# Kernel tuning notes

Measured on AMD Instinct MI355X. Metric: run time of the kernel, lower is better.

The kernel has to match this reference:

```python
import jax, jax.numpy as jnp
import numpy as np

B, S, H, P, D = 4, 2048, 2048, 4096, 1024
I = min(1024, P)  # intermediate_dim


def setup_inputs() -> dict:
    key = jax.random.key(0)
    ks = jax.random.split(key, 8)
    sc = lambda n: 1.0 / np.sqrt(n)
    return {
        "x": jax.random.normal(ks[0], (B, S, H), jnp.float32),
        "tensor_pool": jax.random.normal(ks[1], (P, D), jnp.float32),
        "top_k": 2,
        "w1": jax.random.normal(ks[2], (H, I), jnp.float32) * sc(H),
        "b1": jnp.zeros((I,), jnp.float32),
        "w2": jax.random.normal(ks[3], (I, P), jnp.float32) * sc(I),
        "b2": jnp.zeros((P,), jnp.float32),
        "temperature": jnp.float32(0.5),
        "wp": jax.random.normal(ks[4], (H, D), jnp.float32) * sc(H),
        "bp": jnp.zeros((D,), jnp.float32),
        "gamma": jnp.ones((D,), jnp.float32),
        "beta": jnp.zeros((D,), jnp.float32),
        "wm": jax.random.normal(ks[5], (2 * D, D), jnp.float32) * sc(2 * D),
        "bm": jnp.zeros((D,), jnp.float32),
    }


def _layer_norm(h, gamma, beta, eps=1e-5):
    mu = jnp.mean(h, axis=-1, keepdims=True)
    var = jnp.mean(jnp.square(h - mu), axis=-1, keepdims=True)
    return (h - mu) * jax.lax.rsqrt(var + eps) * gamma + beta


def reference(x, tensor_pool, top_k, w1, b1, w2, b2, temperature, wp, bp, gamma, beta, wm, bm):
    pool_size = tensor_pool.shape[0]
    # router MLP
    inter = jax.nn.relu(jnp.einsum('bsh,hi->bsi', x, w1) + b1)
    logits = jnp.einsum('bsi,ip->bsp', inter, w2) + b2
    temp = jnp.clip(temperature, 0.1, 5.0)
    scaled_logits = jnp.clip(logits / temp, -10.0, 10.0)
    # top-k select + softmax over selected
    topk_logits, topk_idx = jax.lax.top_k(scaled_logits, top_k)  # [B,S,K]
    topk_w = jax.nn.softmax(topk_logits, axis=-1)
    # gather pool entries and combine
    experts_out = tensor_pool[topk_idx]                     # [B,S,K,D]
    weighted_map = jnp.einsum('bsk,bskd->bsd', topk_w, experts_out)
    projected_x = _layer_norm(jnp.einsum('bsh,hd->bsd', x, wp) + bp, gamma, beta)
    combined = jnp.concatenate([projected_x, weighted_map], axis=-1)  # [B,S,2D]
    transformation = jnp.einsum('bse,ed->bsd', combined, wm) + bm
    # usage stats via scatter-add
    usage = jnp.zeros((pool_size,), x.dtype).at[topk_idx.reshape(-1)].add(topk_w.reshape(-1))
    usage_fraction = usage / (usage.sum() + 1e-8)
    uniform = 1.0 / pool_size
    scale = min(1.0, x.size / (pool_size * top_k))
    diversity_loss = jnp.mean(jnp.square(usage_fraction - uniform)) * scale * 0.01
    return transformation, diversity_loss
```

## Files before the change

kernel.cpp:

```cpp
#include <hip/hip_runtime.h>
#include <hip/hip_bf16.h>
#include <float.h>
#include <limits.h>

#define NTOK 8192
#define H_   2048
#define P_   4096
#define D_   1024
#define I_   1024

#define MAXC  16
#define DELTA 0.09375f
#define TAU   4.0e-4f
#define FLAGCAP 512

typedef unsigned short ushort_t;
typedef __attribute__((ext_vector_type(8))) short short8;
typedef __attribute__((ext_vector_type(4))) float floatx4;

static __device__ inline ushort_t f2bf(float f) {
    __hip_bfloat16 h = __float2bfloat16(f);
    return *reinterpret_cast<ushort_t*>(&h);
}
static __device__ inline short f2bfs(float f) {
    __hip_bfloat16 h = __float2bfloat16(f);
    return *reinterpret_cast<short*>(&h);
}
static __device__ inline float bf2f(ushort_t s) { return __uint_as_float((unsigned)s << 16); }

static __device__ inline void ins2(float& v0, int& i0, float& v1, int& i1, float v, int i) {
    if (v > v0 || (v == v0 && i < i0)) { v1 = v0; i1 = i0; v0 = v; i0 = i; }
    else if (v > v1 || (v == v1 && i < i1)) { v1 = v; i1 = i; }
}

static __device__ __forceinline__ void gload16(const void* g, void* l) {
    __builtin_amdgcn_global_load_lds(
        (const __attribute__((address_space(1))) unsigned int*)g,
        (__attribute__((address_space(3))) unsigned int*)l,
        16, 0, 0);
}

__global__ __launch_bounds__(256) void prep_weights(
    const float* __restrict__ w2, float* __restrict__ w2tf, ushort_t* __restrict__ w2t,
    const float* __restrict__ wp, ushort_t* __restrict__ wpt,
    const float* __restrict__ wm, ushort_t* __restrict__ wmt,
    const float* __restrict__ w1, ushort_t* __restrict__ w1tHi, ushort_t* __restrict__ w1tLo)
{
    __shared__ float tile[32][33];
    const int tid = threadIdx.x;
    const int tx = tid & 31, ty = tid >> 5;
    int b = blockIdx.x;
    const float* in; int R, Cc, seg, bx, by;
    if (b < 4096)      { seg = 0; in = w2; R = I_; Cc = P_; bx = b & 127; by = b >> 7; }
    else if (b < 6144) { seg = 1; b -= 4096; in = wp; R = H_; Cc = D_; bx = b & 31; by = b >> 5; }
    else if (b < 8192) { seg = 2; b -= 6144; in = wm; R = H_; Cc = D_; bx = b & 31; by = b >> 5; }
    else               { seg = 3; b -= 8192; in = w1; R = H_; Cc = I_; bx = b & 31; by = b >> 5; }
    const int c0 = bx * 32, r0 = by * 32;
#pragma unroll
    for (int j = 0; j < 4; j++)
        tile[ty + j * 8][tx] = in[(size_t)(r0 + ty + j * 8) * Cc + c0 + tx];
    __syncthreads();
#pragma unroll
    for (int j = 0; j < 4; j++) {
        float v = tile[tx][ty + j * 8];
        const size_t o = (size_t)(c0 + ty + j * 8) * R + r0 + tx;
        if (seg == 0)      { w2t[o] = f2bf(v); w2tf[o] = v; }
        else if (seg == 1) { wpt[o] = f2bf(v); }
        else if (seg == 2) { wmt[o] = f2bf(v); }
        else { ushort_t h = f2bf(v); w1tHi[o] = h; w1tLo[o] = f2bf(v - bf2f(h)); }
    }
}

static __device__ __forceinline__ void stage_slot(
    const ushort_t* __restrict__ base, int ld, int r0, int kt, int p,
    ushort_t* __restrict__ lds)
{
    const int row = p >> 2;
    const int chunk = (p ^ (p >> 2)) & 3;
    gload16(base + (size_t)(r0 + row) * ld + kt * 32 + chunk * 8, lds + p * 8);
}

template<int EPI>
__global__ __launch_bounds__(512, 2) void gemm_pipe(
    const ushort_t* __restrict__ A, int lda,
    const ushort_t* __restrict__ Bt, int ldb,
    const float* __restrict__ bias,
    float* __restrict__ Cf, ushort_t* __restrict__ Cb, int ldc, int K)
{
    __shared__ ushort_t sA[3][256 * 32];
    __shared__ ushort_t sB[3][128 * 32];

    const int tid  = threadIdx.x;
    const int wave = tid >> 6, lane = tid & 63;
    const int lr = lane & 15, lq = lane >> 4;
    const int wrow = wave >> 1, wcol = wave & 1;

    const int nwg = gridDim.x * gridDim.y;
    int bid = blockIdx.y * gridDim.x + blockIdx.x;
    bid = (bid & 7) * (nwg >> 3) + (bid >> 3);
    const int bx = bid % gridDim.x, by = bid / gridDim.x;
    const int m0 = by * 256, n0 = bx * 128;
    const int NT = K >> 5;

    floatx4 acc[4][4] = {};

    stage_slot(A,  lda, m0, 0, tid,       &sA[0][0]);
    stage_slot(A,  lda, m0, 0, tid + 512, &sA[0][0]);
    stage_slot(Bt, ldb, n0, 0, tid,       &sB[0][0]);
    stage_slot(A,  lda, m0, 1, tid,       &sA[1][0]);
    stage_slot(A,  lda, m0, 1, tid + 512, &sA[1][0]);
    stage_slot(Bt, ldb, n0, 1, tid,       &sB[1][0]);

    for (int kt = 0; kt < NT; kt++) {
        const int cb = kt % 3;
        const int sbuf = (kt + 2) % 3;
        const bool st = (kt + 2) < NT;
        const ushort_t* __restrict__ sAc = &sA[cb][0];
        const ushort_t* __restrict__ sBc = &sB[cb][0];
        short8 bF[4];

#pragma unroll
        for (int p = 0; p < 2; p++) {
            if (p == 0) {
                if (kt + 1 < NT) asm volatile("s_waitcnt vmcnt(3)" ::: "memory");
                else             asm volatile("s_waitcnt vmcnt(0)" ::: "memory");
            }
            __builtin_amdgcn_s_barrier();
            short8 aF[2];
#pragma unroll
            for (int t = 0; t < 2; t++) {
                const int row = wrow * 64 + (2 * p + t) * 16 + lr;
                const int ph = row * 4 + (lq ^ (row & 3));
                aF[t] = *(const short8*)&sAc[ph * 8];
            }
            if (p == 0) {
#pragma unroll
                for (int f = 0; f < 4; f++) {
                    const int row = wcol * 64 + f * 16 + lr;
                    const int ph = row * 4 + (lq ^ (row & 3));
                    bF[f] = *(const short8*)&sBc[ph * 8];
                }
            }
            if (st) {
                if (p == 0) {
                    stage_slot(A,  lda, m0, kt + 2, tid, &sA[sbuf][0]);
                    stage_slot(Bt, ldb, n0, kt + 2, tid, &sB[sbuf][0]);
                } else {
                    stage_slot(A,  lda, m0, kt + 2, tid + 512, &sA[sbuf][0]);
                }
            }
            __builtin_amdgcn_s_setprio(1);
#pragma unroll
            for (int t = 0; t < 2; t++)
#pragma unroll
                for (int j = 0; j < 4; j++)
                    acc[2 * p + t][j] = __builtin_amdgcn_mfma_f32_16x16x32_bf16(
                        aF[t], bF[j], acc[2 * p + t][j], 0, 0, 0);
            __builtin_amdgcn_s_setprio(0);
        }
    }

#pragma unroll
    for (int j = 0; j < 4; j++) {
        const int col = n0 + wcol * 64 + j * 16 + lr;
        const float bv = bias[col];
#pragma unroll
        for (int i = 0; i < 4; i++) {
            const int rowb = m0 + wrow * 64 + i * 16 + lq * 4;
#pragma unroll
            for (int r = 0; r < 4; r++) {
                float v = acc[i][j][r] + bv;
                if (EPI == 1) Cb[(size_t)(rowb + r) * ldc + col] = f2bf(v);
                else          Cf[(size_t)(rowb + r) * ldc + col] = v;
            }
        }
    }
}

template<int ASRC, int EPI>
__global__ __launch_bounds__(256) void gemm_lds(
    const void* __restrict__ Av, int lda,
    const ushort_t* __restrict__ Bt, int ldb,
    const float* __restrict__ bias,
    float* __restrict__ Cf, ushort_t* __restrict__ Cb, int ldc, int K)
{
    __shared__ ushort_t sA[128 * 32];
    __shared__ ushort_t sB[128 * 32];

    const int tid  = threadIdx.x;
    const int wave = tid >> 6, lane = tid & 63;
    const int lr = lane & 15, lq = lane >> 4;

    const int nwg = gridDim.x * gridDim.y;
    int bid = blockIdx.y * gridDim.x + blockIdx.x;
    bid = (bid & 7) * (nwg >> 3) + (bid >> 3);
    const int bx = bid % gridDim.x, by = bid / gridDim.x;
    const int m0 = by * 128, n0 = bx * 128;
    const int m0w = m0 + (wave >> 1) * 64, n0w = n0 + (wave & 1) * 64;

    const int n1 = tid, n2 = tid + 256;

    floatx4 acc[4][4] = {};

    for (int k0 = 0; k0 < K; k0 += 32) {
        __syncthreads();
        gload16(Bt + (size_t)(n0 + (n1 >> 2)) * ldb + k0 + (n1 & 3) * 8, &sB[n1 * 8]);
        gload16(Bt + (size_t)(n0 + (n2 >> 2)) * ldb + k0 + (n2 & 3) * 8, &sB[n2 * 8]);
        if (ASRC == 1) {
            const ushort_t* Ab = (const ushort_t*)Av;
            gload16(Ab + (size_t)(m0 + (n1 >> 2)) * lda + k0 + (n1 & 3) * 8, &sA[n1 * 8]);
            gload16(Ab + (size_t)(m0 + (n2 >> 2)) * lda + k0 + (n2 & 3) * 8, &sA[n2 * 8]);
        } else {
#pragma unroll
            for (int ss = 0; ss < 2; ss++) {
                const int s = tid + ss * 256;
                const float* ap = (const float*)Av + (size_t)(m0 + (s >> 2)) * lda + k0 + (s & 3) * 8;
                float4 v0 = *(const float4*)ap;
                float4 v1 = *(const float4*)(ap + 4);
                short8 h;
                h[0] = f2bfs(v0.x); h[1] = f2bfs(v0.y); h[2] = f2bfs(v0.z); h[3] = f2bfs(v0.w);
                h[4] = f2bfs(v1.x); h[5] = f2bfs(v1.y); h[6] = f2bfs(v1.z); h[7] = f2bfs(v1.w);
                *(short8*)&sA[s * 8] = h;
            }
        }
        __syncthreads();

        short8 aF[4], bF[4];
#pragma unroll
        for (int f = 0; f < 4; f++) {
            const int ra = ((wave >> 1) * 64 + f * 16 + lr) * 32 + lq * 8;
            aF[f] = *(const short8*)&sA[ra];
            const int rb = ((wave & 1) * 64 + f * 16 + lr) * 32 + lq * 8;
            bF[f] = *(const short8*)&sB[rb];
        }
#pragma unroll
        for (int i = 0; i < 4; i++)
#pragma unroll
            for (int j = 0; j < 4; j++)
                acc[i][j] = __builtin_amdgcn_mfma_f32_16x16x32_bf16(aF[i], bF[j], acc[i][j], 0, 0, 0);
    }

#pragma unroll
    for (int j = 0; j < 4; j++) {
        const int col = n0w + j * 16 + lr;
        const float bv = bias[col];
#pragma unroll
        for (int i = 0; i < 4; i++) {
            const int rowb = m0w + i * 16 + lq * 4;
#pragma unroll
            for (int r = 0; r < 4; r++) {
                float v = acc[i][j][r] + bv;
                if (EPI == 1) Cb[(size_t)(rowb + r) * ldc + col] = f2bf(v);
                else          Cf[(size_t)(rowb + r) * ldc + col] = v;
            }
        }
    }
}

__global__ __launch_bounds__(256) void gemm_lds_split(
    const float* __restrict__ A, int lda,
    const ushort_t* __restrict__ BtH, const ushort_t* __restrict__ BtL, int ldb,
    const float* __restrict__ bias,
    float* __restrict__ Cf, ushort_t* __restrict__ Cb, int ldc, int K)
{
    __shared__ ushort_t sAh[128 * 32];
    __shared__ ushort_t sAl[128 * 32];
    __shared__ ushort_t sBh[128 * 32];
    __shared__ ushort_t sBl[128 * 32];

    const int tid  = threadIdx.x;
    const int wave = tid >> 6, lane = tid & 63;
    const int lr = lane & 15, lq = lane >> 4;

    const int nwg = gridDim.x * gridDim.y;
    int bid = blockIdx.y * gridDim.x + blockIdx.x;
    bid = (bid & 7) * (nwg >> 3) + (bid >> 3);
    const int bx = bid % gridDim.x, by = bid / gridDim.x;
    const int m0 = by * 128, n0 = bx * 128;
    const int m0w = m0 + (wave >> 1) * 64, n0w = n0 + (wave & 1) * 64;

    const int n1 = tid, n2 = tid + 256;

    floatx4 acc[4][4] = {};

    for (int k0 = 0; k0 < K; k0 += 32) {
        __syncthreads();
        gload16(BtH + (size_t)(n0 + (n1 >> 2)) * ldb + k0 + (n1 & 3) * 8, &sBh[n1 * 8]);
        gload16(BtH + (size_t)(n0 + (n2 >> 2)) * ldb + k0 + (n2 & 3) * 8, &sBh[n2 * 8]);
        gload16(BtL + (size_t)(n0 + (n1 >> 2)) * ldb + k0 + (n1 & 3) * 8, &sBl[n1 * 8]);
        gload16(BtL + (size_t)(n0 + (n2 >> 2)) * ldb + k0 + (n2 & 3) * 8, &sBl[n2 * 8]);
#pragma unroll
        for (int ss = 0; ss < 2; ss++) {
            const int s = tid + ss * 256;
            const float* ap = A + (size_t)(m0 + (s >> 2)) * lda + k0 + (s & 3) * 8;
            float4 v0 = *(const float4*)ap;
            float4 v1 = *(const float4*)(ap + 4);
            float fb[8] = {v0.x, v0.y, v0.z, v0.w, v1.x, v1.y, v1.z, v1.w};
            short8 h, l;
#pragma unroll
            for (int e = 0; e < 8; e++) {
                short hh = f2bfs(fb[e]);
                h[e] = hh; l[e] = f2bfs(fb[e] - bf2f((ushort_t)hh));
            }
            *(short8*)&sAh[s * 8] = h;
            *(short8*)&sAl[s * 8] = l;
        }
        __syncthreads();

        short8 aH[4], aL[4], bH[4], bL[4];
#pragma unroll
        for (int f = 0; f < 4; f++) {
            const int ra = ((wave >> 1) * 64 + f * 16 + lr) * 32 + lq * 8;
            aH[f] = *(const short8*)&sAh[ra];
            aL[f] = *(const short8*)&sAl[ra];
            const int rb = ((wave & 1) * 64 + f * 16 + lr) * 32 + lq * 8;
            bH[f] = *(const short8*)&sBh[rb];
            bL[f] = *(const short8*)&sBl[rb];
        }
#pragma unroll
        for (int i = 0; i < 4; i++)
#pragma unroll
            for (int j = 0; j < 4; j++) {
                acc[i][j] = __builtin_amdgcn_mfma_f32_16x16x32_bf16(aH[i], bH[j], acc[i][j], 0, 0, 0);
                acc[i][j] = __builtin_amdgcn_mfma_f32_16x16x32_bf16(aH[i], bL[j], acc[i][j], 0, 0, 0);
                acc[i][j] = __builtin_amdgcn_mfma_f32_16x16x32_bf16(aL[i], bH[j], acc[i][j], 0, 0, 0);
            }
    }

#pragma unroll
    for (int j = 0; j < 4; j++) {
        const int col = n0w + j * 16 + lr;
        const float bv = bias[col];
#pragma unroll
        for (int i = 0; i < 4; i++) {
            const int rowb = m0w + i * 16 + lq * 4;
#pragma unroll
            for (int r = 0; r < 4; r++) {
                float v = fmaxf(acc[i][j][r] + bv, 0.f);
                Cf[(size_t)(rowb + r) * ldc + col] = v;
                Cb[(size_t)(rowb + r) * ldc + col] = f2bf(v);
            }
        }
    }
}

__global__ __launch_bounds__(256) void cand_scan(
    const ushort_t* __restrict__ logitsb,
    int* __restrict__ cidx, int* __restrict__ ccnt)
{
    __shared__ float sv0[4], sv1[4];
    __shared__ int   scnt;
    const int tok = blockIdx.x;
    const int tid = threadIdx.x;
    const ushort_t* row = logitsb + (size_t)tok * P_;

    float my[16];
    {
        const uint4* rp = (const uint4*)(row + tid * 16);
        uint4 u0 = rp[0], u1 = rp[1];
        unsigned w[8] = {u0.x, u0.y, u0.z, u0.w, u1.x, u1.y, u1.z, u1.w};
#pragma unroll
        for (int j = 0; j < 8; j++) {
            my[2 * j]     = __uint_as_float(w[j] << 16);
            my[2 * j + 1] = __uint_as_float(w[j] & 0xFFFF0000u);
        }
    }
    float v0 = -FLT_MAX, v1 = -FLT_MAX;
#pragma unroll
    for (int j = 0; j < 16; j++) {
        float v = my[j];
        if (v > v0) { v1 = v0; v0 = v; } else if (v > v1) v1 = v;
    }
#pragma unroll
    for (int off = 1; off < 64; off <<= 1) {
        float u0 = __shfl_xor(v0, off), u1 = __shfl_xor(v1, off);
        float n0 = fmaxf(v0, u0);
        float n1 = fmaxf(fminf(v0, u0), fmaxf(v1, u1));
        v0 = n0; v1 = n1;
    }
    const int wv = tid >> 6;
    if ((tid & 63) == 0) { sv0[wv] = v0; sv1[wv] = v1; }
    if (tid == 0) scnt = 0;
    __syncthreads();
    float g0 = -FLT_MAX, g1 = -FLT_MAX;
#pragma unroll
    for (int w = 0; w < 4; w++) {
        float u0 = sv0[w], u1 = sv1[w];
        float n0 = fmaxf(g0, u0);
        float n1 = fmaxf(fminf(g0, u0), fmaxf(g1, u1));
        g0 = n0; g1 = n1;
    }
    const float thresh = g1 - DELTA;
#pragma unroll
    for (int j = 0; j < 16; j++) {
        if (my[j] >= thresh) {
            int pos = atomicAdd(&scnt, 1);
            if (pos < MAXC) cidx[tok * MAXC + pos] = tid * 16 + j;
        }
    }
    __syncthreads();
    if (tid == 0) ccnt[tok] = min(scnt, MAXC);
}

__global__ __launch_bounds__(256) void recheck(
    const float* __restrict__ interf, const float* __restrict__ w2tf,
    const float* __restrict__ b2, const int* __restrict__ cidx,
    const int* __restrict__ ccnt, const float* __restrict__ temp_p,
    int2* __restrict__ tki, float2* __restrict__ tkw,
    int* __restrict__ flagcnt, int* __restrict__ flaglist)
{
    __shared__ double ex[MAXC];
    __shared__ int    sidx[MAXC];
    const int tok  = blockIdx.x;
    const int tid  = threadIdx.x;
    const int wave = tid >> 6, lane = tid & 63;
    int cnt = min(max(ccnt[tok], 0), MAXC);

    const float* ir = interf + (size_t)tok * I_;
    for (int c = wave; c < cnt; c += 4) {
        int p = min(max(cidx[tok * MAXC + c], 0), P_ - 1);
        const float* wr = w2tf + (size_t)p * I_;
        double s = 0.0;
        for (int k = lane; k < I_; k += 64)
            s += (double)ir[k] * (double)wr[k];
#pragma unroll
        for (int off = 32; off; off >>= 1) s += __shfl_down(s, off);
        if (lane == 0) { ex[c] = s + (double)b2[p]; sidx[c] = p; }
    }
    __syncthreads();
    if (tid == 0) {
        float v0 = -FLT_MAX, v1 = -FLT_MAX; int i0 = INT_MAX, i1 = INT_MAX;
        for (int c = 0; c < cnt; c++) ins2(v0, i0, v1, i1, (float)ex[c], sidx[c]);
        if (i0 == INT_MAX) { i0 = 0; v0 = 0.f; }
        if (i1 == INT_MAX) { i1 = i0; v1 = v0; }
        if (cnt >= 3) {
            float v2 = -FLT_MAX;
            for (int c = 0; c < cnt; c++) {
                if (sidx[c] == i0 || sidx[c] == i1) continue;
                float v = (float)ex[c];
                if (v > v2) v2 = v;
            }
            if (v1 - v2 < TAU) {
                int pos = atomicAdd(flagcnt, 1);
                if (pos < FLAGCAP) flaglist[pos] = tok;
            }
        }
        float tc = fminf(fmaxf(temp_p[0], 0.1f), 5.0f);
        float s0 = fminf(fmaxf(v0 / tc, -10.f), 10.f);
        float s1 = fminf(fmaxf(v1 / tc, -10.f), 10.f);
        float m  = fmaxf(s0, s1);
        float e0 = expf(s0 - m), e1 = expf(s1 - m);
        float inv = 1.0f / (e0 + e1);
        tki[tok] = make_int2(i0, i1);
        tkw[tok] = make_float2(e0 * inv, e1 * inv);
    }
}

__global__ __launch_bounds__(256) void fallback_gemv(
    const float* __restrict__ x, const float* __restrict__ w1,
    const int* __restrict__ flagcnt, const int* __restrict__ flaglist,
    double* __restrict__ part)
{
    __shared__ float sx[128];
    const int tid = threadIdx.x;
    const int nf = min(flagcnt[0], FLAGCAP);
    const int nitems = nf * 16;

    for (int idx = blockIdx.x; idx < nitems; idx += gridDim.x) {
        const int fi = idx >> 4, slice = idx & 15;
        const int tok = flaglist[fi];
        const int h0 = slice * 128;
        __syncthreads();
        if (tid < 128) sx[tid] = x[(size_t)tok * H_ + h0 + tid];
        __syncthreads();

        const int col = tid * 4;
        double a0 = 0.0, a1 = 0.0, a2 = 0.0, a3 = 0.0;
        for (int h = 0; h < 128; h += 8) {
            float4 wv[8];
#pragma unroll
            for (int u = 0; u < 8; u++)
                wv[u] = *(const float4*)(w1 + (size_t)(h0 + h + u) * I_ + col);
#pragma unroll
            for (int u = 0; u < 8; u++) {
                const double xv = (double)sx[h + u];
                a0 += xv * (double)wv[u].x;
                a1 += xv * (double)wv[u].y;
                a2 += xv * (double)wv[u].z;
                a3 += xv * (double)wv[u].w;
            }
        }
        double* pp = part + ((size_t)fi * 16 + slice) * I_ + col;
        pp[0] = a0; pp[1] = a1; pp[2] = a2; pp[3] = a3;
    }
}

__global__ __launch_bounds__(256) void fallback_reduce(
    const double* __restrict__ part, const float* __restrict__ b1,
    const float* __restrict__ w2tf, const float* __restrict__ b2,
    const int* __restrict__ cidx, const int* __restrict__ ccnt,
    const int* __restrict__ flagcnt, const int* __restrict__ flaglist,
    const float* __restrict__ temp_p,
    int2* __restrict__ tki, float2* __restrict__ tkw)
{
    __shared__ double sInter[I_];
    __shared__ double ex[MAXC];
    __shared__ int    sidx[MAXC];
    const int tid  = threadIdx.x;
    const int wave = tid >> 6, lane = tid & 63;
    const int nf = min(flagcnt[0], FLAGCAP);

    for (int fi = blockIdx.x; fi < nf; fi += gridDim.x) {
        const int tok = flaglist[fi];
        __syncthreads();
#pragma unroll
        for (int q = 0; q < 4; q++) {
            const int i = q * 256 + tid;
            double v = (double)b1[i];
            const double* pp = part + (size_t)fi * 16 * I_ + i;
#pragma unroll
            for (int s = 0; s < 16; s++) v += pp[(size_t)s * I_];
            sInter[i] = v > 0.0 ? v : 0.0;
        }
        __syncthreads();

        const int cnt = min(max(ccnt[tok], 0), MAXC);
        for (int c = wave; c < cnt; c += 4) {
            int p = min(max(cidx[tok * MAXC + c], 0), P_ - 1);
            const float* wr = w2tf + (size_t)p * I_;
            double s = 0.0;
            for (int k = lane; k < I_; k += 64)
                s += sInter[k] * (double)wr[k];
#pragma unroll
            for (int off = 32; off; off >>= 1) s += __shfl_down(s, off);
            if (lane == 0) { ex[c] = s + (double)b2[p]; sidx[c] = p; }
        }
        __syncthreads();
        if (tid == 0) {
            float v0 = -FLT_MAX, v1 = -FLT_MAX; int i0 = INT_MAX, i1 = INT_MAX;
            for (int c = 0; c < cnt; c++) ins2(v0, i0, v1, i1, (float)ex[c], sidx[c]);
            if (i0 == INT_MAX) { i0 = 0; v0 = 0.f; }
            if (i1 == INT_MAX) { i1 = i0; v1 = v0; }
            float tc = fminf(fmaxf(temp_p[0], 0.1f), 5.0f);
            float s0 = fminf(fmaxf(v0 / tc, -10.f), 10.f);
            float s1 = fminf(fmaxf(v1 / tc, -10.f), 10.f);
            float m  = fmaxf(s0, s1);
            float e0 = expf(s0 - m), e1 = expf(s1 - m);
            float inv = 1.0f / (e0 + e1);
            tki[tok] = make_int2(i0, i1);
            tkw[tok] = make_float2(e0 * inv, e1 * inv);
        }
    }
}

static __device__ inline float blockReduceSum256(float v, float* red) {
#pragma unroll
    for (int off = 32; off; off >>= 1) v += __shfl_down(v, off);
    const int wv = threadIdx.x >> 6;
    if ((threadIdx.x & 63) == 0) red[wv] = v;
    __syncthreads();
    float tot = red[0] + red[1] + red[2] + red[3];
    __syncthreads();
    return tot;
}

__global__ __launch_bounds__(256) void build_combined(
    const float* __restrict__ proj, ushort_t* __restrict__ comb,
    const float* __restrict__ pool,
    const float* __restrict__ gamma, const float* __restrict__ beta,
    const int2* __restrict__ tki, const float2* __restrict__ tkw,
    float* __restrict__ usage)
{
    __shared__ float red[4];
    const int tok = blockIdx.x;
    const int tid = threadIdx.x;
    const int c = tid * 4;

    float4 v = *(const float4*)&proj[(size_t)tok * D_ + c];
    float s = v.x + v.y + v.z + v.w;
    float tot = blockReduceSum256(s, red);
    float mu = tot * (1.0f / D_);
    float d0 = v.x - mu, d1 = v.y - mu, d2 = v.z - mu, d3 = v.w - mu;
    float sq = d0 * d0 + d1 * d1 + d2 * d2 + d3 * d3;
    float var = blockReduceSum256(sq, red) * (1.0f / D_);
    float rs = 1.0f / sqrtf(var + 1e-5f);

    float4 g  = *(const float4*)&gamma[c];
    float4 be = *(const float4*)&beta[c];
    ushort4 o;
    o.x = f2bf(d0 * rs * g.x + be.x);
    o.y = f2bf(d1 * rs * g.y + be.y);
    o.z = f2bf(d2 * rs * g.z + be.z);
    o.w = f2bf(d3 * rs * g.w + be.w);
    *(ushort4*)&comb[(size_t)tok * (2 * D_) + c] = o;

    int2   ii = tki[tok];
    int ia = min(max(ii.x, 0), P_ - 1);
    int ib = min(max(ii.y, 0), P_ - 1);
    float2 ww = tkw[tok];
    float4 p0 = *(const float4*)&pool[(size_t)ia * D_ + c];
    float4 p1 = *(const float4*)&pool[(size_t)ib * D_ + c];
    ushort4 wm;
    wm.x = f2bf(ww.x * p0.x + ww.y * p1.x);
    wm.y = f2bf(ww.x * p0.y + ww.y * p1.y);
    wm.z = f2bf(ww.x * p0.z + ww.y * p1.z);
    wm.w = f2bf(ww.x * p0.w + ww.y * p1.w);
    *(ushort4*)&comb[(size_t)tok * (2 * D_) + D_ + c] = wm;

    if (tid == 0) {
        atomicAdd(&usage[ia], ww.x);
        atomicAdd(&usage[ib], ww.y);
    }
}

__global__ __launch_bounds__(256) void diversity_kernel(
    const float* __restrict__ usage, float* __restrict__ out)
{
    __shared__ float red[4];
    const int tid = threadIdx.x;
    float s = 0.f;
    for (int j = tid; j < P_; j += 256) s += usage[j];
    float tot = blockReduceSum256(s, red) + 1e-8f;
    float q = 0.f;
    const float uni = 1.0f / P_;
    for (int j = tid; j < P_; j += 256) {
        float f = usage[j] / tot - uni;
        q += f * f;
    }
    float ssq = blockReduceSum256(q, red);
    if (tid == 0) out[(size_t)NTOK * D_] = ssq * (1.0f / P_) * 0.01f;
}

extern "C" void kernel_launch(void* const* d_in, const int* in_sizes, int n_in,
                              void* d_out, int out_size, void* d_ws, size_t ws_size,
                              hipStream_t stream) {
    const float* x     = (const float*)d_in[0];
    const float* pool  = (const float*)d_in[1];
    const float* w1    = (const float*)d_in[3];
    const float* b1    = (const float*)d_in[4];
    const float* w2    = (const float*)d_in[5];
    const float* b2    = (const float*)d_in[6];
    const float* temp  = (const float*)d_in[7];
    const float* wp    = (const float*)d_in[8];
    const float* bp    = (const float*)d_in[9];
    const float* gamma = (const float*)d_in[10];
    const float* beta  = (const float*)d_in[11];
    const float* wm    = (const float*)d_in[12];
    const float* bm    = (const float*)d_in[13];
    float* out = (float*)d_out;

    float* ws = (float*)d_ws;
    const size_t MF = (size_t)1024 * 1024;
    float*    interf  = ws;
    ushort_t* interb  = (ushort_t*)(ws + 8 * MF);
    ushort_t* logitsb = (ushort_t*)(ws + 12 * MF);
    double*   part    = (double*)(ws + 12 * MF);
    float*    projb   = ws + 12 * MF;
    ushort_t* comb    = (ushort_t*)(ws + 20 * MF);
    float*    w2tf    = ws + 28 * MF;
    ushort_t* w2t     = (ushort_t*)(ws + 32 * MF);
    ushort_t* wpt     = (ushort_t*)(ws + 34 * MF);
    ushort_t* wmt     = (ushort_t*)(ws + 35 * MF);
    ushort_t* w1tHi   = (ushort_t*)(ws + 36 * MF);
    ushort_t* w1tLo   = (ushort_t*)(ws + 37 * MF);
    int*      cidx    = (int*)(ws + 38 * MF);
    int*      ccnt    = cidx + NTOK * MAXC;
    int2*     tki     = (int2*)(ccnt + NTOK);
    float2*   tkw     = (float2*)(tki + NTOK);
    float*    usage   = (float*)(tkw + NTOK);
    int*      flagcnt = (int*)(usage + P_);
    int*      flaglist= flagcnt + 1;

    hipMemsetAsync(usage, 0, (P_ + 1) * sizeof(float), stream);

    dim3 blk(256);
    prep_weights<<<10240, blk, 0, stream>>>(w2, w2tf, w2t, wp, wpt, wm, wmt,
                                            w1, w1tHi, w1tLo);

    gemm_lds_split<<<dim3(I_ / 128, NTOK / 128), blk, 0, stream>>>(
        x, H_, w1tHi, w1tLo, H_, b1, interf, interb, I_, H_);

    gemm_pipe<1><<<dim3(P_ / 128, NTOK / 256), dim3(512), 0, stream>>>(
        interb, I_, w2t, I_, b2, nullptr, logitsb, P_, I_);

    cand_scan<<<NTOK, blk, 0, stream>>>(logitsb, cidx, ccnt);
    recheck<<<NTOK, blk, 0, stream>>>(interf, w2tf, b2, cidx, ccnt, temp, tki, tkw,
                                      flagcnt, flaglist);

    fallback_gemv<<<1024, blk, 0, stream>>>(x, w1, flagcnt, flaglist, part);
    fallback_reduce<<<128, blk, 0, stream>>>(part, b1, w2tf, b2, cidx, ccnt,
                                             flagcnt, flaglist, temp, tki, tkw);

    gemm_lds<0, 0><<<dim3(D_ / 128, NTOK / 128), blk, 0, stream>>>(
        x, H_, wpt, H_, bp, projb, nullptr, D_, H_);

    build_combined<<<NTOK, blk, 0, stream>>>(projb, comb, pool, gamma, beta, tki, tkw, usage);

    gemm_pipe<0><<<dim3(D_ / 128, NTOK / 256), dim3(512), 0, stream>>>(
        comb, 2 * D_, wmt, 2 * D_, bm, out, nullptr, D_, 2 * D_);

    diversity_kernel<<<1, blk, 0, stream>>>(usage, out);
}
```

Baseline: 563.7 us.

## Pre-split x into bf16 hi/lo and use pipelined split GEMM for router layer

```diff
diff --git a/kernel.cpp b/kernel.cpp
--- a/kernel.cpp
+++ b/kernel.cpp
@@ -38,6 +38,24 @@
         (const __attribute__((address_space(1))) unsigned int*)g,
         (__attribute__((address_space(3))) unsigned int*)l,
         16, 0, 0);
+}
+
+__global__ __launch_bounds__(256) void split_x(
+    const float* __restrict__ in, ushort_t* __restrict__ hi,
+    ushort_t* __restrict__ lo, int n4)
+{
+    int idx = blockIdx.x * 256 + threadIdx.x;
+    const int stride = gridDim.x * 256;
+    for (; idx < n4; idx += stride) {
+        float4 v = ((const float4*)in)[idx];
+        ushort4 h, l;
+        h.x = f2bf(v.x); l.x = f2bf(v.x - bf2f(h.x));
+        h.y = f2bf(v.y); l.y = f2bf(v.y - bf2f(h.y));
+        h.z = f2bf(v.z); l.z = f2bf(v.z - bf2f(h.z));
+        h.w = f2bf(v.w); l.w = f2bf(v.w - bf2f(h.w));
+        ((ushort4*)hi)[idx] = h;
+        ((ushort4*)lo)[idx] = l;
+    }
 }
 
 __global__ __launch_bounds__(256) void prep_weights(
@@ -177,6 +195,119 @@
     }
 }
 
+__global__ __launch_bounds__(512, 2) void gemm_pipe_split(
+    const ushort_t* __restrict__ AH, const ushort_t* __restrict__ AL, int lda,
+    const ushort_t* __restrict__ BtH, const ushort_t* __restrict__ BtL, int ldb,
+    const float* __restrict__ bias,
+    float* __restrict__ Cf, ushort_t* __restrict__ Cb, int ldc, int K)
+{
+    __shared__ ushort_t sAh[3][256 * 32];
+    __shared__ ushort_t sAl[3][256 * 32];
+    __shared__ ushort_t sBh[3][128 * 32];
+    __shared__ ushort_t sBl[3][128 * 32];
+
+    const int tid  = threadIdx.x;
+    const int wave = tid >> 6, lane = tid & 63;
+    const int lr = lane & 15, lq = lane >> 4;
+    const int wrow = wave >> 1, wcol = wave & 1;
+
+    const int nwg = gridDim.x * gridDim.y;
+    int bid = blockIdx.y * gridDim.x + blockIdx.x;
+    bid = (bid & 7) * (nwg >> 3) + (bid >> 3);
+    const int bx = bid % gridDim.x, by = bid / gridDim.x;
+    const int m0 = by * 256, n0 = bx * 128;
+    const int NT = K >> 5;
+
+    floatx4 acc[4][4] = {};
+
+#pragma unroll
+    for (int t = 0; t < 2; t++) {
+        stage_slot(AH,  lda, m0, t, tid,       &sAh[t][0]);
+        stage_slot(AH,  lda, m0, t, tid + 512, &sAh[t][0]);
+        stage_slot(AL,  lda, m0, t, tid,       &sAl[t][0]);
+        stage_slot(AL,  lda, m0, t, tid + 512, &sAl[t][0]);
+        stage_slot(BtH, ldb, n0, t, tid,       &sBh[t][0]);
+        stage_slot(BtL, ldb, n0, t, tid,       &sBl[t][0]);
+    }
+
+    for (int kt = 0; kt < NT; kt++) {
+        const int cb = kt % 3;
+        const int sbuf = (kt + 2) % 3;
+        const bool st = (kt + 2) < NT;
+        const ushort_t* __restrict__ sAhc = &sAh[cb][0];
+        const ushort_t* __restrict__ sAlc = &sAl[cb][0];
+        const ushort_t* __restrict__ sBhc = &sBh[cb][0];
+        const ushort_t* __restrict__ sBlc = &sBl[cb][0];
+        short8 bH[4], bL[4];
+
+#pragma unroll
+        for (int p = 0; p < 2; p++) {
+            if (p == 0) {
+                if (kt + 1 < NT) asm volatile("s_waitcnt vmcnt(6)" ::: "memory");
+                else             asm volatile("s_waitcnt vmcnt(0)" ::: "memory");
+            }
+            __builtin_amdgcn_s_barrier();
+            short8 aH[2], aL[2];
+#pragma unroll
+            for (int t = 0; t < 2; t++) {
+                const int row = wrow * 64 + (2 * p + t) * 16 + lr;
+                const int ph = (row * 4 + (lq ^ (row & 3))) * 8;
+                aH[t] = *(const short8*)&sAhc[ph];
+                aL[t] = *(const short8*)&sAlc[ph];
+            }
+            if (p == 0) {
+#pragma unroll
+                for (int f = 0; f < 4; f++) {
+                    const int row = wcol * 64 + f * 16 + lr;
+                    const int ph = (row * 4 + (lq ^ (row & 3))) * 8;
+                    bH[f] = *(const short8*)&sBhc[ph];
+                    bL[f] = *(const short8*)&sBlc[ph];
+                }
+            }
+            if (st) {
+                if (p == 0) {
+                    stage_slot(AH,  lda, m0, kt + 2, tid, &sAh[sbuf][0]);
+                    stage_slot(AL,  lda, m0, kt + 2, tid, &sAl[sbuf][0]);
+                    stage_slot(BtH, ldb, n0, kt + 2, tid, &sBh[sbuf][0]);
+                } else {
+                    stage_slot(AH,  lda, m0, kt + 2, tid + 512, &sAh[sbuf][0]);
+                    stage_slot(AL,  lda, m0, kt + 2, tid + 512, &sAl[sbuf][0]);
+                    stage_slot(BtL, ldb, n0, kt + 2, tid, &sBl[sbuf][0]);
+                }
+            }
+            __builtin_amdgcn_s_setprio(1);
+#pragma unroll
+            for (int t = 0; t < 2; t++)
+#pragma unroll
+                for (int j = 0; j < 4; j++) {
+                    acc[2 * p + t][j] = __builtin_amdgcn_mfma_f32_16x16x32_bf16(
+                        aH[t], bH[j], acc[2 * p + t][j], 0, 0, 0);
+                    acc[2 * p + t][j] = __builtin_amdgcn_mfma_f32_16x16x32_bf16(
+                        aH[t], bL[j], acc[2 * p + t][j], 0, 0, 0);
+                    acc[2 * p + t][j] = __builtin_amdgcn_mfma_f32_16x16x32_bf16(
+                        aL[t], bH[j], acc[2 * p + t][j], 0, 0, 0);
+                }
+            __builtin_amdgcn_s_setprio(0);
+        }
+    }
+
+#pragma unroll
+    for (int j = 0; j < 4; j++) {
+        const int col = n0 + wcol * 64 + j * 16 + lr;
+        const float bv = bias[col];
+#pragma unroll
+        for (int i = 0; i < 4; i++) {
+            const int rowb = m0 + wrow * 64 + i * 16 + lq * 4;
+#pragma unroll
+            for (int r = 0; r < 4; r++) {
+                float v = fmaxf(acc[i][j][r] + bv, 0.f);
+                Cf[(size_t)(rowb + r) * ldc + col] = v;
+                Cb[(size_t)(rowb + r) * ldc + col] = f2bf(v);
+            }
+        }
+    }
+}
+
 template<int ASRC, int EPI>
 __global__ __launch_bounds__(256) void gemm_lds(
     const void* __restrict__ Av, int lda,
@@ -252,93 +383,6 @@
                 float v = acc[i][j][r] + bv;
                 if (EPI == 1) Cb[(size_t)(rowb + r) * ldc + col] = f2bf(v);
                 else          Cf[(size_t)(rowb + r) * ldc + col] = v;
-            }
-        }
-    }
-}
-
-__global__ __launch_bounds__(256) void gemm_lds_split(
-    const float* __restrict__ A, int lda,
-    const ushort_t* __restrict__ BtH, const ushort_t* __restrict__ BtL, int ldb,
-    const float* __restrict__ bias,
-    float* __restrict__ Cf, ushort_t* __restrict__ Cb, int ldc, int K)
-{
-    __shared__ ushort_t sAh[128 * 32];
-    __shared__ ushort_t sAl[128 * 32];
-    __shared__ ushort_t sBh[128 * 32];
-    __shared__ ushort_t sBl[128 * 32];
-
-    const int tid  = threadIdx.x;
-    const int wave = tid >> 6, lane = tid & 63;
-    const int lr = lane & 15, lq = lane >> 4;
-
-    const int nwg = gridDim.x * gridDim.y;
-    int bid = blockIdx.y * gridDim.x + blockIdx.x;
-    bid = (bid & 7) * (nwg >> 3) + (bid >> 3);
-    const int bx = bid % gridDim.x, by = bid / gridDim.x;
-    const int m0 = by * 128, n0 = bx * 128;
-    const int m0w = m0 + (wave >> 1) * 64, n0w = n0 + (wave & 1) * 64;
-
-    const int n1 = tid, n2 = tid + 256;
-
-    floatx4 acc[4][4] = {};
-
-    for (int k0 = 0; k0 < K; k0 += 32) {
-        __syncthreads();
-        gload16(BtH + (size_t)(n0 + (n1 >> 2)) * ldb + k0 + (n1 & 3) * 8, &sBh[n1 * 8]);
-        gload16(BtH + (size_t)(n0 + (n2 >> 2)) * ldb + k0 + (n2 & 3) * 8, &sBh[n2 * 8]);
-        gload16(BtL + (size_t)(n0 + (n1 >> 2)) * ldb + k0 + (n1 & 3) * 8, &sBl[n1 * 8]);
-        gload16(BtL + (size_t)(n0 + (n2 >> 2)) * ldb + k0 + (n2 & 3) * 8, &sBl[n2 * 8]);
-#pragma unroll
-        for (int ss = 0; ss < 2; ss++) {
-            const int s = tid + ss * 256;
-            const float* ap = A + (size_t)(m0 + (s >> 2)) * lda + k0 + (s & 3) * 8;
-            float4 v0 = *(const float4*)ap;
-            float4 v1 = *(const float4*)(ap + 4);
-            float fb[8] = {v0.x, v0.y, v0.z, v0.w, v1.x, v1.y, v1.z, v1.w};
-            short8 h, l;
-#pragma unroll
-            for (int e = 0; e < 8; e++) {
-                short hh = f2bfs(fb[e]);
-                h[e] = hh; l[e] = f2bfs(fb[e] - bf2f((ushort_t)hh));
-            }
-            *(short8*)&sAh[s * 8] = h;
-            *(short8*)&sAl[s * 8] = l;
-        }
-        __syncthreads();
-
-        short8 aH[4], aL[4], bH[4], bL[4];
-#pragma unroll
-        for (int f = 0; f < 4; f++) {
-            const int ra = ((wave >> 1) * 64 + f * 16 + lr) * 32 + lq * 8;
-            aH[f] = *(const short8*)&sAh[ra];
-            aL[f] = *(const short8*)&sAl[ra];
-            const int rb = ((wave & 1) * 64 + f * 16 + lr) * 32 + lq * 8;
-            bH[f] = *(const short8*)&sBh[rb];
-            bL[f] = *(const short8*)&sBl[rb];
-        }
-#pragma unroll
-        for (int i = 0; i < 4; i++)
-#pragma unroll
-            for (int j = 0; j < 4; j++) {
-                acc[i][j] = __builtin_amdgcn_mfma_f32_16x16x32_bf16(aH[i], bH[j], acc[i][j], 0, 0, 0);
-                acc[i][j] = __builtin_amdgcn_mfma_f32_16x16x32_bf16(aH[i], bL[j], acc[i][j], 0, 0, 0);
-                acc[i][j] = __builtin_amdgcn_mfma_f32_16x16x32_bf16(aL[i], bH[j], acc[i][j], 0, 0, 0);
-            }
-    }
-
-#pragma unroll
-    for (int j = 0; j < 4; j++) {
-        const int col = n0w + j * 16 + lr;
-        const float bv = bias[col];
-#pragma unroll
-        for (int i = 0; i < 4; i++) {
-            const int rowb = m0w + i * 16 + lq * 4;
-#pragma unroll
-            for (int r = 0; r < 4; r++) {
-                float v = fmaxf(acc[i][j][r] + bv, 0.f);
-                Cf[(size_t)(rowb + r) * ldc + col] = v;
-                Cb[(size_t)(rowb + r) * ldc + col] = f2bf(v);
             }
         }
     }
@@ -653,6 +697,8 @@
     const size_t MF = (size_t)1024 * 1024;
     float*    interf  = ws;
     ushort_t* interb  = (ushort_t*)(ws + 8 * MF);
+    ushort_t* xHi     = (ushort_t*)(ws + 12 * MF);
+    ushort_t* xLo     = (ushort_t*)(ws + 20 * MF);
     ushort_t* logitsb = (ushort_t*)(ws + 12 * MF);
     double*   part    = (double*)(ws + 12 * MF);
     float*    projb   = ws + 12 * MF;
@@ -677,8 +723,10 @@
     prep_weights<<<10240, blk, 0, stream>>>(w2, w2tf, w2t, wp, wpt, wm, wmt,
                                             w1, w1tHi, w1tLo);
 
-    gemm_lds_split<<<dim3(I_ / 128, NTOK / 128), blk, 0, stream>>>(
-        x, H_, w1tHi, w1tLo, H_, b1, interf, interb, I_, H_);
+    split_x<<<2048, blk, 0, stream>>>(x, xHi, xLo, NTOK * H_ / 4);
+
+    gemm_pipe_split<<<dim3(I_ / 128, NTOK / 256), dim3(512), 0, stream>>>(
+        xHi, xLo, H_, w1tHi, w1tLo, H_, b1, interf, interb, I_, H_);
 
     gemm_pipe<1><<<dim3(P_ / 128, NTOK / 256), dim3(512), 0, stream>>>(
         interb, I_, w2t, I_, b2, nullptr, logitsb, P_, I_);
```

Result: slower. 591.6 us (+5.0%).
